# Kernel optimization log

Measured on AMD Instinct MI355X. Metric: run time of the kernel, lower is better.

Reference implementation:

```python
import jax, jax.numpy as jnp
import numpy as np

N_NODES = 20000
N_EDGES = 320000
IN_FEATS = 64
HIDDENS = [128, 128, 128]
K = 4        # n_kernels
DIM = 2      # pseudo_coord


def setup_inputs() -> dict:
    key = jax.random.key(0)
    ks = jax.random.split(key, 32)
    inp = {
        "features": jax.random.normal(ks[0], (N_NODES, IN_FEATS), dtype=jnp.float32),
        "pseudo": jax.random.uniform(ks[1], (N_EDGES, DIM), dtype=jnp.float32),
        "src": jax.random.randint(ks[2], (N_EDGES,), 0, N_NODES, dtype=jnp.int32),
        "dst": jax.random.randint(ks[3], (N_EDGES,), 0, N_NODES, dtype=jnp.int32),
    }
    dims_in = [IN_FEATS] + HIDDENS[:-1]
    ki = 4
    for i, (din, dout) in enumerate(zip(dims_in, HIDDENS)):
        inp[f"fc_w{i}"] = jax.random.normal(ks[ki], (din, K * dout), dtype=jnp.float32) * (1.0 / np.sqrt(din)); ki += 1
        inp[f"mu{i}"] = jax.random.normal(ks[ki], (K, DIM), dtype=jnp.float32) * 0.1; ki += 1
        inp[f"inv_sigma{i}"] = jnp.ones((K, DIM), dtype=jnp.float32)
        inp[f"bias{i}"] = jnp.zeros((dout,), dtype=jnp.float32)
        inp[f"pw{i}"] = jax.random.normal(ks[ki], (DIM, DIM), dtype=jnp.float32) * 0.5; ki += 1
        inp[f"pb{i}"] = jnp.zeros((DIM,), dtype=jnp.float32)
    return inp


def _gmm_layer(h, pseudo, src, dst, fc_w, mu, inv_sigma, bias, pw, pb):
    k, dim = mu.shape
    dout = fc_w.shape[1] // k
    hp = (h @ fc_w).reshape(-1, k, dout)              # [N, K, out]
    u = jnp.tanh(pseudo @ pw + pb)                    # [E, dim] per-layer pseudo projection
    diff = (u[:, None, :] - mu[None, :, :]) * inv_sigma[None, :, :]
    w = jnp.exp(-0.5 * jnp.sum(diff * diff, axis=-1))  # [E, K] Gaussian mixture weights
    msg = jnp.einsum('ek,eko->eo', w, hp[src])         # gather + weighted mix -> [E, out]
    agg = jax.ops.segment_sum(msg, dst, num_segments=h.shape[0])  # scatter-sum
    return agg + bias


def reference(features, pseudo, src, dst,
              fc_w0, mu0, inv_sigma0, bias0, pw0, pb0,
              fc_w1, mu1, inv_sigma1, bias1, pw1, pb1,
              fc_w2, mu2, inv_sigma2, bias2, pw2, pb2):
    h = features
    h = _gmm_layer(h, pseudo, src, dst, fc_w0, mu0, inv_sigma0, bias0, pw0, pb0)
    h = _gmm_layer(h, pseudo, src, dst, fc_w1, mu1, inv_sigma1, bias1, pw1, pb1)
    h = _gmm_layer(h, pseudo, src, dst, fc_w2, mu2, inv_sigma2, bias2, pw2, pb2)
    return h
```

## Files before the change

### kernel.cpp

```cpp
#include <hip/hip_runtime.h>
#include <hip/hip_bf16.h>
#include <math.h>

#define NN 20000
#define NE 320000

typedef __attribute__((ext_vector_type(8))) short bf16x8;
typedef __attribute__((ext_vector_type(4))) float f32x4;

__device__ inline float bf2f_lo(uint v) {
    union { uint i; float f; } c; c.i = v << 16; return c.f;
}
__device__ inline float bf2f_hi(uint v) {
    union { uint i; float f; } c; c.i = v & 0xffff0000u; return c.f;
}
__device__ inline ushort f2bf(float f) {
    __hip_bfloat16 h = __float2bfloat16(f);
    return *reinterpret_cast<ushort*>(&h);
}

__global__ void count_kernel(const int* __restrict__ dst, int* __restrict__ counts) {
    int e = blockIdx.x * blockDim.x + threadIdx.x;
    if (e < NE) atomicAdd(&counts[dst[e]], 1);
}

__global__ __launch_bounds__(1024) void scan_kernel(const int* __restrict__ counts,
                                                    int* __restrict__ offsets,
                                                    int* __restrict__ cursor) {
    __shared__ int part[1024];
    const int T = 1024, CHK = (NN + T - 1) / T;
    int t = threadIdx.x;
    int begin = t * CHK;
    int end = begin + CHK < NN ? begin + CHK : NN;
    int s = 0;
    for (int i = begin; i < end; ++i) s += counts[i];
    part[t] = s;
    __syncthreads();
    for (int off = 1; off < T; off <<= 1) {
        int v = (t >= off) ? part[t - off] : 0;
        __syncthreads();
        part[t] += v;
        __syncthreads();
    }
    int run = (t == 0) ? 0 : part[t - 1];
    for (int i = begin; i < end; ++i) {
        offsets[i] = run;
        cursor[i] = run;
        run += counts[i];
    }
    if (t == T - 1) offsets[NN] = part[T - 1];
}

__global__ void fill1_kernel(const int* __restrict__ dst, int* __restrict__ cursor,
                             int* __restrict__ csr_eidx) {
    int e = blockIdx.x * blockDim.x + threadIdx.x;
    if (e >= NE) return;
    int pos = atomicAdd(&cursor[dst[e]], 1);
    csr_eidx[pos] = e;
}

struct EdgeParams {
    const float *pw0, *pb0, *mu0, *is0;
    const float *pw1, *pb1, *mu1, *is1;
    const float *pw2, *pb2, *mu2, *is2;
};

__device__ inline float fast_tanh(float x) {
    x = fminf(fmaxf(x, -9.f), 9.f);
    float e = __expf(2.f * x);
    return 1.f - 2.f / (e + 1.f);
}

__device__ inline void layer_w(float p0, float p1, const float* pw, const float* pb,
                               const float* mu, const float* is, float* out4) {
    float u0 = fast_tanh(p0 * pw[0] + p1 * pw[2] + pb[0]);
    float u1 = fast_tanh(p0 * pw[1] + p1 * pw[3] + pb[1]);
#pragma unroll
    for (int k = 0; k < 4; ++k) {
        float d0 = (u0 - mu[k * 2 + 0]) * is[k * 2 + 0];
        float d1 = (u1 - mu[k * 2 + 1]) * is[k * 2 + 1];
        out4[k] = __expf(-0.5f * (d0 * d0 + d1 * d1));
    }
}

__global__ void fill2_prep(const int* __restrict__ csr_eidx, const int* __restrict__ src,
                           const float* __restrict__ pseudo, EdgeParams P,
                           int* __restrict__ csr_src, float* __restrict__ csr_w,
                           const float* __restrict__ f0, const float* __restrict__ f1,
                           const float* __restrict__ f2, ushort* __restrict__ w0,
                           ushort* __restrict__ w1, ushort* __restrict__ w2) {
    int bid = blockIdx.x;
    if (bid < 1250) {
        int i = bid * 256 + threadIdx.x;
        int e = csr_eidx[i];
        float2 p = *(const float2*)(pseudo + (size_t)e * 2);
        csr_src[i] = src[e];
        float w[4];
        layer_w(p.x, p.y, P.pw0, P.pb0, P.mu0, P.is0, w);
        *(float4*)(csr_w + (size_t)(0 * NE + i) * 4) = make_float4(w[0], w[1], w[2], w[3]);
        layer_w(p.x, p.y, P.pw1, P.pb1, P.mu1, P.is1, w);
        *(float4*)(csr_w + (size_t)(1 * NE + i) * 4) = make_float4(w[0], w[1], w[2], w[3]);
        layer_w(p.x, p.y, P.pw2, P.pb2, P.mu2, P.is2, w);
        *(float4*)(csr_w + (size_t)(2 * NE + i) * 4) = make_float4(w[0], w[1], w[2], w[3]);
    } else {
        int idx = (bid - 1250) * 256 + threadIdx.x;
        const float* srcp;
        ushort* dstp;
        int din, KD, li;
        if (idx < 128 * 256) {
            srcp = f0; dstp = w0; din = 64; KD = 256; li = idx;
        } else if (idx < 128 * 256 + 128 * 512) {
            srcp = f1; dstp = w1; din = 128; KD = 512; li = idx - 128 * 256;
        } else {
            srcp = f2; dstp = w2; din = 128; KD = 512; li = idx - 128 * 256 - 128 * 512;
        }
        int n = li / KD;
        int r = li - n * KD;
        int k = r / din;
        int d = r - k * din;
        dstp[li] = f2bf(srcp[d * 512 + k * 128 + n]);
    }
}

template <int DIN, bool INF32, bool OUTBF>
__global__ __launch_bounds__(256, 4) void layer_fused(const void* __restrict__ hin,
                                                      const int* __restrict__ offsets,
                                                      const int* __restrict__ csr_src,
                                                      const float* __restrict__ csr_w,
                                                      const ushort* __restrict__ Bt,
                                                      const float* __restrict__ bias,
                                                      void* __restrict__ hout) {
    constexpr int KD = 4 * DIN;
    constexpr int PITCH = KD + 8;
    __shared__ __align__(16) ushort Ts[16 * PITCH];
    int wv = threadIdx.x >> 6, lane = threadIdx.x & 63;
    int l16 = lane & 15, quad = lane >> 4;
    int nb = blockIdx.x * 16;
    const float4* wp = (const float4*)csr_w;

#pragma unroll
    for (int j = 0; j < 4; ++j) {
        int row = wv * 4 + j;
        int n = nb + row;
        int b = __builtin_amdgcn_readfirstlane(offsets[n]);
        int e = __builtin_amdgcn_readfirstlane(offsets[n + 1]);
        if (INF32) {
            const float* h = (const float*)hin;
            float a0 = 0.f, a1 = 0.f, a2 = 0.f, a3 = 0.f;
            int i = b;
            for (; i + 8 <= e; i += 8) {
                int s[8]; float4 w[8]; float hv[8];
#pragma unroll
                for (int u = 0; u < 8; ++u) s[u] = csr_src[i + u];
#pragma unroll
                for (int u = 0; u < 8; ++u) w[u] = wp[i + u];
#pragma unroll
                for (int u = 0; u < 8; ++u) hv[u] = h[(size_t)s[u] * 64 + lane];
#pragma unroll
                for (int u = 0; u < 8; ++u) {
                    a0 += w[u].x * hv[u];
                    a1 += w[u].y * hv[u];
                    a2 += w[u].z * hv[u];
                    a3 += w[u].w * hv[u];
                }
            }
            if (i < e) {
                int s[8]; float4 w[8]; float hv[8];
#pragma unroll
                for (int u = 0; u < 8; ++u) {
                    int ii = i + u;
                    bool val = ii < e;
                    int idx = val ? ii : b;
                    s[u] = csr_src[idx];
                    float4 t = wp[idx];
                    w[u] = val ? t : make_float4(0.f, 0.f, 0.f, 0.f);
                }
#pragma unroll
                for (int u = 0; u < 8; ++u) hv[u] = h[(size_t)s[u] * 64 + lane];
#pragma unroll
                for (int u = 0; u < 8; ++u) {
                    a0 += w[u].x * hv[u];
                    a1 += w[u].y * hv[u];
                    a2 += w[u].z * hv[u];
                    a3 += w[u].w * hv[u];
                }
            }
            Ts[row * PITCH + 0 * 64 + lane] = f2bf(a0);
            Ts[row * PITCH + 1 * 64 + lane] = f2bf(a1);
            Ts[row * PITCH + 2 * 64 + lane] = f2bf(a2);
            Ts[row * PITCH + 3 * 64 + lane] = f2bf(a3);
        } else {
            const ushort* h = (const ushort*)hin;
            float a00 = 0.f, a01 = 0.f, a10 = 0.f, a11 = 0.f;
            float a20 = 0.f, a21 = 0.f, a30 = 0.f, a31 = 0.f;
            int i = b;
            for (; i + 8 <= e; i += 8) {
                int s[8]; float4 w[8]; uint v[8];
#pragma unroll
                for (int u = 0; u < 8; ++u) s[u] = csr_src[i + u];
#pragma unroll
                for (int u = 0; u < 8; ++u) w[u] = wp[i + u];
#pragma unroll
                for (int u = 0; u < 8; ++u)
                    v[u] = *(const uint*)(h + (size_t)s[u] * DIN + lane * 2);
#pragma unroll
                for (int u = 0; u < 8; ++u) {
                    float lo = bf2f_lo(v[u]), hi = bf2f_hi(v[u]);
                    a00 += w[u].x * lo; a01 += w[u].x * hi;
                    a10 += w[u].y * lo; a11 += w[u].y * hi;
                    a20 += w[u].z * lo; a21 += w[u].z * hi;
                    a30 += w[u].w * lo; a31 += w[u].w * hi;
                }
            }
            if (i < e) {
                int s[8]; float4 w[8]; uint v[8];
#pragma unroll
                for (int u = 0; u < 8; ++u) {
                    int ii = i + u;
                    bool val = ii < e;
                    int idx = val ? ii : b;
                    s[u] = csr_src[idx];
                    float4 t = wp[idx];
                    w[u] = val ? t : make_float4(0.f, 0.f, 0.f, 0.f);
                }
#pragma unroll
                for (int u = 0; u < 8; ++u)
                    v[u] = *(const uint*)(h + (size_t)s[u] * DIN + lane * 2);
#pragma unroll
                for (int u = 0; u < 8; ++u) {
                    float lo = bf2f_lo(v[u]), hi = bf2f_hi(v[u]);
                    a00 += w[u].x * lo; a01 += w[u].x * hi;
                    a10 += w[u].y * lo; a11 += w[u].y * hi;
                    a20 += w[u].z * lo; a21 += w[u].z * hi;
                    a30 += w[u].w * lo; a31 += w[u].w * hi;
                }
            }
            ushort2 p;
            p.x = f2bf(a00); p.y = f2bf(a01);
            *(ushort2*)(Ts + row * PITCH + 0 * DIN + lane * 2) = p;
            p.x = f2bf(a10); p.y = f2bf(a11);
            *(ushort2*)(Ts + row * PITCH + 1 * DIN + lane * 2) = p;
            p.x = f2bf(a20); p.y = f2bf(a21);
            *(ushort2*)(Ts + row * PITCH + 2 * DIN + lane * 2) = p;
            p.x = f2bf(a30); p.y = f2bf(a31);
            *(ushort2*)(Ts + row * PITCH + 3 * DIN + lane * 2) = p;
        }
    }
    __syncthreads();

    f32x4 acc[2];
    acc[0] = (f32x4){0.f, 0.f, 0.f, 0.f};
    acc[1] = (f32x4){0.f, 0.f, 0.f, 0.f};
#pragma unroll 4
    for (int k0 = 0; k0 < KD; k0 += 32) {
        bf16x8 af = *(const bf16x8*)(Ts + l16 * PITCH + k0 + quad * 8);
#pragma unroll
        for (int c = 0; c < 2; ++c) {
            int nr = wv * 32 + c * 16 + l16;
            bf16x8 bfr = *(const bf16x8*)(Bt + (size_t)nr * KD + k0 + quad * 8);
            acc[c] = __builtin_amdgcn_mfma_f32_16x16x32_bf16(af, bfr, acc[c], 0, 0, 0);
        }
    }
#pragma unroll
    for (int c = 0; c < 2; ++c) {
        int gn = wv * 32 + c * 16 + l16;
        float bv = bias[gn];
#pragma unroll
        for (int i = 0; i < 4; ++i) {
            int gm = nb + quad * 4 + i;
            float val = acc[c][i] + bv;
            if (OUTBF)
                ((ushort*)hout)[(size_t)gm * 128 + gn] = f2bf(val);
            else
                ((float*)hout)[(size_t)gm * 128 + gn] = val;
        }
    }
}

extern "C" void kernel_launch(void* const* d_in, const int* in_sizes, int n_in,
                              void* d_out, int out_size, void* d_ws, size_t ws_size,
                              hipStream_t stream) {
    const float* features = (const float*)d_in[0];
    const float* pseudo = (const float*)d_in[1];
    const int* src = (const int*)d_in[2];
    const int* dst = (const int*)d_in[3];
    const float* fc_w[3] = {(const float*)d_in[4], (const float*)d_in[10], (const float*)d_in[16]};
    const float* mu[3] = {(const float*)d_in[5], (const float*)d_in[11], (const float*)d_in[17]};
    const float* isg[3] = {(const float*)d_in[6], (const float*)d_in[12], (const float*)d_in[18]};
    const float* bias[3] = {(const float*)d_in[7], (const float*)d_in[13], (const float*)d_in[19]};
    const float* pw[3] = {(const float*)d_in[8], (const float*)d_in[14], (const float*)d_in[20]};
    const float* pb[3] = {(const float*)d_in[9], (const float*)d_in[15], (const float*)d_in[21]};

    char* ws = (char*)d_ws;
    auto alloc = [&](size_t bytes) -> void* {
        void* p = (void*)ws;
        ws += (bytes + 255) & ~(size_t)255;
        return p;
    };
    int* counts = (int*)alloc((size_t)NN * 4);
    int* offsets = (int*)alloc((size_t)(NN + 1) * 4);
    int* cursor = (int*)alloc((size_t)NN * 4);
    int* csr_eidx = (int*)alloc((size_t)NE * 4);
    int* csr_src = (int*)alloc((size_t)NE * 4);
    float* csr_w = (float*)alloc((size_t)3 * NE * 4 * 4);
    ushort* w2t_0 = (ushort*)alloc((size_t)128 * 256 * 2);
    ushort* w2t_1 = (ushort*)alloc((size_t)128 * 512 * 2);
    ushort* w2t_2 = (ushort*)alloc((size_t)128 * 512 * 2);
    ushort* h1 = (ushort*)alloc((size_t)NN * 128 * 2);
    ushort* h2 = (ushort*)alloc((size_t)NN * 128 * 2);

    hipMemsetAsync(counts, 0, (size_t)NN * 4, stream);
    count_kernel<<<(NE + 255) / 256, 256, 0, stream>>>(dst, counts);
    scan_kernel<<<1, 1024, 0, stream>>>(counts, offsets, cursor);
    fill1_kernel<<<(NE + 255) / 256, 256, 0, stream>>>(dst, cursor, csr_eidx);

    EdgeParams P;
    P.pw0 = pw[0]; P.pb0 = pb[0]; P.mu0 = mu[0]; P.is0 = isg[0];
    P.pw1 = pw[1]; P.pb1 = pb[1]; P.mu1 = mu[1]; P.is1 = isg[1];
    P.pw2 = pw[2]; P.pb2 = pb[2]; P.mu2 = mu[2]; P.is2 = isg[2];
    fill2_prep<<<1890, 256, 0, stream>>>(csr_eidx, src, pseudo, P, csr_src, csr_w,
                                         fc_w[0], fc_w[1], fc_w[2], w2t_0, w2t_1, w2t_2);

    const int GB = NN / 16;

    layer_fused<64, true, true><<<GB, 256, 0, stream>>>(
        features, offsets, csr_src, csr_w + (size_t)0 * NE * 4, w2t_0, bias[0], h1);
    layer_fused<128, false, true><<<GB, 256, 0, stream>>>(
        h1, offsets, csr_src, csr_w + (size_t)1 * NE * 4, w2t_1, bias[1], h2);
    layer_fused<128, false, false><<<GB, 256, 0, stream>>>(
        h2, offsets, csr_src, csr_w + (size_t)2 * NE * 4, w2t_2, bias[2], (float*)d_out);
}
```

Measured before the change: 264.7 us.

## Store edge mixture weights as fp16, widen gather batch, vectorize scan

Per-edge Gaussian weights are packed into fp16 (8 bytes per edge instead of 16) and unpacked in the aggregation loop, halving the bytes written in prep and read per layer. The aggregation loop now takes 16 edges per iteration with masking in place of an 8-wide main loop plus a separate tail, giving more loads in flight. The single-block scan caches counts in registers and uses int4 loads and stores. The cost is fp16 rounding of the weights, more registers per thread, and wasted masked slots for low-degree nodes.

```diff
diff --git a/kernel.cpp b/kernel.cpp
--- a/kernel.cpp
+++ b/kernel.cpp
@@ -1,5 +1,6 @@
 #include <hip/hip_runtime.h>
 #include <hip/hip_bf16.h>
+#include <hip/hip_fp16.h>
 #include <math.h>
 
 #define NN 20000
@@ -16,6 +17,14 @@
 }
 __device__ inline ushort f2bf(float f) {
     __hip_bfloat16 h = __float2bfloat16(f);
+    return *reinterpret_cast<ushort*>(&h);
+}
+__device__ inline float2 h2f2(uint u) {
+    union { uint i; __half2 h; } c; c.i = u;
+    return __half22float2(c.h);
+}
+__device__ inline ushort f2h(float f) {
+    __half h = __float2half_rn(f);
     return *reinterpret_cast<ushort*>(&h);
 }
 
@@ -31,9 +40,26 @@
     const int T = 1024, CHK = (NN + T - 1) / T;
     int t = threadIdx.x;
     int begin = t * CHK;
-    int end = begin + CHK < NN ? begin + CHK : NN;
+    int c[CHK];
     int s = 0;
-    for (int i = begin; i < end; ++i) s += counts[i];
+    bool full = (begin + CHK <= NN);
+    if (full) {
+#pragma unroll
+        for (int q = 0; q < CHK / 4; ++q) {
+            int4 v = *(const int4*)(counts + begin + q * 4);
+            c[q * 4 + 0] = v.x; c[q * 4 + 1] = v.y; c[q * 4 + 2] = v.z; c[q * 4 + 3] = v.w;
+        }
+#pragma unroll
+        for (int q = 0; q < CHK; ++q) s += c[q];
+    } else {
+        int end = begin + CHK < NN ? begin + CHK : NN;
+        if (begin > NN) begin = NN;
+        for (int i = begin; i < end; ++i) {
+            int v = counts[i];
+            c[i - begin] = v;
+            s += v;
+        }
+    }
     part[t] = s;
     __syncthreads();
     for (int off = 1; off < T; off <<= 1) {
@@ -43,10 +69,24 @@
         __syncthreads();
     }
     int run = (t == 0) ? 0 : part[t - 1];
-    for (int i = begin; i < end; ++i) {
-        offsets[i] = run;
-        cursor[i] = run;
-        run += counts[i];
+    if (full) {
+#pragma unroll
+        for (int q = 0; q < CHK / 4; ++q) {
+            int4 o;
+            o.x = run; run += c[q * 4 + 0];
+            o.y = run; run += c[q * 4 + 1];
+            o.z = run; run += c[q * 4 + 2];
+            o.w = run; run += c[q * 4 + 3];
+            *(int4*)(offsets + begin + q * 4) = o;
+            *(int4*)(cursor + begin + q * 4) = o;
+        }
+    } else {
+        int end = begin + CHK < NN ? begin + CHK : NN;
+        for (int i = begin; i < end; ++i) {
+            offsets[i] = run;
+            cursor[i] = run;
+            run += c[i - begin];
+        }
     }
     if (t == T - 1) offsets[NN] = part[T - 1];
 }
@@ -85,7 +125,7 @@
 
 __global__ void fill2_prep(const int* __restrict__ csr_eidx, const int* __restrict__ src,
                            const float* __restrict__ pseudo, EdgeParams P,
-                           int* __restrict__ csr_src, float* __restrict__ csr_w,
+                           int* __restrict__ csr_src, ushort* __restrict__ csr_w,
                            const float* __restrict__ f0, const float* __restrict__ f1,
                            const float* __restrict__ f2, ushort* __restrict__ w0,
                            ushort* __restrict__ w1, ushort* __restrict__ w2) {
@@ -96,12 +136,19 @@
         float2 p = *(const float2*)(pseudo + (size_t)e * 2);
         csr_src[i] = src[e];
         float w[4];
+        uint2 pk;
         layer_w(p.x, p.y, P.pw0, P.pb0, P.mu0, P.is0, w);
-        *(float4*)(csr_w + (size_t)(0 * NE + i) * 4) = make_float4(w[0], w[1], w[2], w[3]);
+        pk.x = (uint)f2h(w[0]) | ((uint)f2h(w[1]) << 16);
+        pk.y = (uint)f2h(w[2]) | ((uint)f2h(w[3]) << 16);
+        *(uint2*)(csr_w + (size_t)(0 * NE + i) * 4) = pk;
         layer_w(p.x, p.y, P.pw1, P.pb1, P.mu1, P.is1, w);
-        *(float4*)(csr_w + (size_t)(1 * NE + i) * 4) = make_float4(w[0], w[1], w[2], w[3]);
+        pk.x = (uint)f2h(w[0]) | ((uint)f2h(w[1]) << 16);
+        pk.y = (uint)f2h(w[2]) | ((uint)f2h(w[3]) << 16);
+        *(uint2*)(csr_w + (size_t)(1 * NE + i) * 4) = pk;
         layer_w(p.x, p.y, P.pw2, P.pb2, P.mu2, P.is2, w);
-        *(float4*)(csr_w + (size_t)(2 * NE + i) * 4) = make_float4(w[0], w[1], w[2], w[3]);
+        pk.x = (uint)f2h(w[0]) | ((uint)f2h(w[1]) << 16);
+        pk.y = (uint)f2h(w[2]) | ((uint)f2h(w[3]) << 16);
+        *(uint2*)(csr_w + (size_t)(2 * NE + i) * 4) = pk;
     } else {
         int idx = (bid - 1250) * 256 + threadIdx.x;
         const float* srcp;
@@ -126,17 +173,17 @@
 __global__ __launch_bounds__(256, 4) void layer_fused(const void* __restrict__ hin,
                                                       const int* __restrict__ offsets,
                                                       const int* __restrict__ csr_src,
-                                                      const float* __restrict__ csr_w,
+                                                      const ushort* __restrict__ csr_w,
                                                       const ushort* __restrict__ Bt,
                                                       const float* __restrict__ bias,
                                                       void* __restrict__ hout) {
     constexpr int KD = 4 * DIN;
     constexpr int PITCH = KD + 8;
+    constexpr int BATCH = 16;
     __shared__ __align__(16) ushort Ts[16 * PITCH];
     int wv = threadIdx.x >> 6, lane = threadIdx.x & 63;
     int l16 = lane & 15, quad = lane >> 4;
     int nb = blockIdx.x * 16;
-    const float4* wp = (const float4*)csr_w;
 
 #pragma unroll
     for (int j = 0; j < 4; ++j) {
@@ -147,42 +194,28 @@
         if (INF32) {
             const float* h = (const float*)hin;
             float a0 = 0.f, a1 = 0.f, a2 = 0.f, a3 = 0.f;
-            int i = b;
-            for (; i + 8 <= e; i += 8) {
-                int s[8]; float4 w[8]; float hv[8];
-#pragma unroll
-                for (int u = 0; u < 8; ++u) s[u] = csr_src[i + u];
-#pragma unroll
-                for (int u = 0; u < 8; ++u) w[u] = wp[i + u];
-#pragma unroll
-                for (int u = 0; u < 8; ++u) hv[u] = h[(size_t)s[u] * 64 + lane];
-#pragma unroll
-                for (int u = 0; u < 8; ++u) {
-                    a0 += w[u].x * hv[u];
-                    a1 += w[u].y * hv[u];
-                    a2 += w[u].z * hv[u];
-                    a3 += w[u].w * hv[u];
+            for (int i = b; i < e; i += BATCH) {
+                int s[BATCH]; uint wlo[BATCH], whi[BATCH]; float hv[BATCH];
+#pragma unroll
+                for (int u = 0; u < BATCH; ++u) {
+                    int ii = i + u;
+                    bool ok = ii < e;
+                    int idx = ok ? ii : b;
+                    s[u] = csr_src[idx];
+                    uint2 wp = *(const uint2*)(csr_w + (size_t)idx * 4);
+                    wlo[u] = ok ? wp.x : 0u;
+                    whi[u] = ok ? wp.y : 0u;
                 }
-            }
-            if (i < e) {
-                int s[8]; float4 w[8]; float hv[8];
-#pragma unroll
-                for (int u = 0; u < 8; ++u) {
-                    int ii = i + u;
-                    bool val = ii < e;
-                    int idx = val ? ii : b;
-                    s[u] = csr_src[idx];
-                    float4 t = wp[idx];
-                    w[u] = val ? t : make_float4(0.f, 0.f, 0.f, 0.f);
-                }
-#pragma unroll
-                for (int u = 0; u < 8; ++u) hv[u] = h[(size_t)s[u] * 64 + lane];
-#pragma unroll
-                for (int u = 0; u < 8; ++u) {
-                    a0 += w[u].x * hv[u];
-                    a1 += w[u].y * hv[u];
-                    a2 += w[u].z * hv[u];
-                    a3 += w[u].w * hv[u];
+#pragma unroll
+                for (int u = 0; u < BATCH; ++u) hv[u] = h[(size_t)s[u] * 64 + lane];
+#pragma unroll
+                for (int u = 0; u < BATCH; ++u) {
+                    float2 wa = h2f2(wlo[u]);
+                    float2 wb = h2f2(whi[u]);
+                    a0 += wa.x * hv[u];
+                    a1 += wa.y * hv[u];
+                    a2 += wb.x * hv[u];
+                    a3 += wb.y * hv[u];
                 }
             }
             Ts[row * PITCH + 0 * 64 + lane] = f2bf(a0);
@@ -193,46 +226,30 @@
             const ushort* h = (const ushort*)hin;
             float a00 = 0.f, a01 = 0.f, a10 = 0.f, a11 = 0.f;
             float a20 = 0.f, a21 = 0.f, a30 = 0.f, a31 = 0.f;
-            int i = b;
-            for (; i + 8 <= e; i += 8) {
-                int s[8]; float4 w[8]; uint v[8];
-#pragma unroll
-                for (int u = 0; u < 8; ++u) s[u] = csr_src[i + u];
-#pragma unroll
-                for (int u = 0; u < 8; ++u) w[u] = wp[i + u];
-#pragma unroll
-                for (int u = 0; u < 8; ++u)
+            for (int i = b; i < e; i += BATCH) {
+                int s[BATCH]; uint wlo[BATCH], whi[BATCH]; uint v[BATCH];
+#pragma unroll
+                for (int u = 0; u < BATCH; ++u) {
+                    int ii = i + u;
+                    bool ok = ii < e;
+                    int idx = ok ? ii : b;
+                    s[u] = csr_src[idx];
+                    uint2 wp = *(const uint2*)(csr_w + (size_t)idx * 4);
+                    wlo[u] = ok ? wp.x : 0u;
+                    whi[u] = ok ? wp.y : 0u;
+                }
+#pragma unroll
+                for (int u = 0; u < BATCH; ++u)
                     v[u] = *(const uint*)(h + (size_t)s[u] * DIN + lane * 2);
 #pragma unroll
-                for (int u = 0; u < 8; ++u) {
+                for (int u = 0; u < BATCH; ++u) {
+                    float2 wa = h2f2(wlo[u]);
+                    float2 wb = h2f2(whi[u]);
                     float lo = bf2f_lo(v[u]), hi = bf2f_hi(v[u]);
-                    a00 += w[u].x * lo; a01 += w[u].x * hi;
-                    a10 += w[u].y * lo; a11 += w[u].y * hi;
-                    a20 += w[u].z * lo; a21 += w[u].z * hi;
-                    a30 += w[u].w * lo; a31 += w[u].w * hi;
-                }
-            }
-            if (i < e) {
-                int s[8]; float4 w[8]; uint v[8];
-#pragma unroll
-                for (int u = 0; u < 8; ++u) {
-                    int ii = i + u;
-                    bool val = ii < e;
-                    int idx = val ? ii : b;
-                    s[u] = csr_src[idx];
-                    float4 t = wp[idx];
-                    w[u] = val ? t : make_float4(0.f, 0.f, 0.f, 0.f);
-                }
-#pragma unroll
-                for (int u = 0; u < 8; ++u)
-                    v[u] = *(const uint*)(h + (size_t)s[u] * DIN + lane * 2);
-#pragma unroll
-                for (int u = 0; u < 8; ++u) {
-                    float lo = bf2f_lo(v[u]), hi = bf2f_hi(v[u]);
-                    a00 += w[u].x * lo; a01 += w[u].x * hi;
-                    a10 += w[u].y * lo; a11 += w[u].y * hi;
-                    a20 += w[u].z * lo; a21 += w[u].z * hi;
-                    a30 += w[u].w * lo; a31 += w[u].w * hi;
+                    a00 += wa.x * lo; a01 += wa.x * hi;
+                    a10 += wa.y * lo; a11 += wa.y * hi;
+                    a20 += wb.x * lo; a21 += wb.x * hi;
+                    a30 += wb.y * lo; a31 += wb.y * hi;
                 }
             }
             ushort2 p;
@@ -302,7 +319,7 @@
     int* cursor = (int*)alloc((size_t)NN * 4);
     int* csr_eidx = (int*)alloc((size_t)NE * 4);
     int* csr_src = (int*)alloc((size_t)NE * 4);
-    float* csr_w = (float*)alloc((size_t)3 * NE * 4 * 4);
+    ushort* csr_w = (ushort*)alloc((size_t)3 * NE * 4 * 2);
     ushort* w2t_0 = (ushort*)alloc((size_t)128 * 256 * 2);
     ushort* w2t_1 = (ushort*)alloc((size_t)128 * 512 * 2);
     ushort* w2t_2 = (ushort*)alloc((size_t)128 * 512 * 2);
```

New measurement: 267.8 us. Within noise of the previous version (+1.2%).
